# Optimization experiments

Measured on AMD Instinct MI355X. Metric: run time of the kernel, lower is better.

Reference implementation:

```python
import jax, jax.numpy as jnp
import numpy as np

B, NC, PY, PX = 1, 2, 32, 32
DIM, HEADS = 1024, 16
IMAGE_H = IMAGE_W = 448
FREQ_BASE = 100.0


def _so3_exp(w):
    # w: (..., 3) axis-angle -> (..., 3, 3) rotation (Rodrigues)
    theta = jnp.maximum(jnp.linalg.norm(w, axis=-1, keepdims=True)[..., None], 1e-8)
    wx, wy, wz = w[..., 0], w[..., 1], w[..., 2]
    z = jnp.zeros_like(wx)
    K = jnp.stack([jnp.stack([z, -wz, wy], -1),
                   jnp.stack([wz, z, -wx], -1),
                   jnp.stack([-wy, wx, z], -1)], -2)
    A = jnp.sin(theta) / theta
    Bc = (1.0 - jnp.cos(theta)) / (theta * theta)
    return jnp.eye(3) + A * K + Bc * (K @ K)


def setup_inputs() -> dict:
    key = jax.random.key(0)
    ks = jax.random.split(key, 6)
    N = NC * PY * PX
    x = jax.random.normal(ks[0], (B, N, DIM), jnp.float32)
    # SE(3) camera extrinsics (world-to-camera)
    R = _so3_exp(0.2 * jax.random.normal(ks[1], (B, NC, 3), jnp.float32))
    t = 0.5 * jax.random.normal(ks[2], (B, NC, 3), jnp.float32)
    ext = jnp.zeros((B, NC, 4, 4), jnp.float32)
    ext = ext.at[..., :3, :3].set(R).at[..., :3, 3].set(t).at[..., 3, 3].set(1.0)
    f = 500.0
    Ks = jnp.zeros((B, NC, 3, 3), jnp.float32)
    Ks = (Ks.at[..., 0, 0].set(f).at[..., 1, 1].set(f)
            .at[..., 0, 2].set(IMAGE_W / 2.0).at[..., 1, 2].set(IMAGE_H / 2.0)
            .at[..., 2, 2].set(1.0))
    s = 1.0 / np.sqrt(DIM)
    qkv_w = s * jax.random.normal(ks[3], (3 * DIM, DIM), jnp.float32)
    proj_w = s * jax.random.normal(ks[4], (DIM, DIM), jnp.float32)
    proj_b = jnp.zeros((DIM,), jnp.float32)
    return dict(x=x, extrinsics=ext, Ks=Ks, qkv_w=qkv_w, proj_w=proj_w, proj_b=proj_b,
                image_h=IMAGE_H, image_w=IMAGE_W, patch_h=PY, patch_w=PX)


def _prope_attention(x, extrinsics, Ks, qkv_w, proj_w, proj_b,
                     image_h, image_w, patch_h, patch_w):
    Bb, N, C = x.shape
    H = HEADS
    D = C // H
    nc = extrinsics.shape[1]
    n_per = patch_h * patch_w  # tokens per camera

    # ---- QKV projection ----
    qkv = (x @ qkv_w.T).reshape(Bb, N, 3, H, D).transpose(0, 3, 2, 1, 4)  # B,H,3,N,D
    q, k, v = qkv[:, :, 0], qkv[:, :, 1], qkv[:, :, 2]

    # ---- per-camera normalized projection matrices P = K_norm(4x4) @ viewmat ----
    sx, sy = 2.0 / image_w, 2.0 / image_h  # pixel -> NDC-ish normalization
    Kn = jnp.zeros(Ks.shape[:-2] + (4, 4), x.dtype)
    Kn = (Kn.at[..., 0, 0].set(Ks[..., 0, 0] * sx)
            .at[..., 1, 1].set(Ks[..., 1, 1] * sy)
            .at[..., 0, 2].set(Ks[..., 0, 2] * sx - 1.0)
            .at[..., 1, 2].set(Ks[..., 1, 2] * sy - 1.0)
            .at[..., 2, 2].set(1.0).at[..., 3, 3].set(1.0))
    P = Kn @ extrinsics                      # (B, nc, 4, 4)
    P_inv = jnp.linalg.inv(P)

    def per_token(M):  # (B,nc,4,4) -> (B,N,4,4), broadcast camera over its tokens
        return jnp.repeat(M, n_per, axis=1)

    Mq = per_token(jnp.swapaxes(P_inv, -1, -2))  # P_i^{-T}
    Mk = per_token(P)                            # P_j
    Mo = per_token(P_inv)                        # P_i^{-1}

    # ---- channel split: half projective (blocks of 4), half 2D RoPE ----
    d_proj = D // 2
    d_rope = D - d_proj
    nf = d_rope // 4  # frequencies per axis (pairs of channels)
    freqs = FREQ_BASE ** (-jnp.arange(nf, dtype=x.dtype) / nf)
    ysg, xsg = jnp.meshgrid(jnp.arange(patch_h), jnp.arange(patch_w), indexing='ij')
    pos_x = jnp.tile(xsg.reshape(-1), nc).astype(x.dtype)  # (N,)
    pos_y = jnp.tile(ysg.reshape(-1), nc).astype(x.dtype)
    ang = jnp.concatenate([pos_x[:, None] * freqs, pos_y[:, None] * freqs], -1)  # (N, 2nf)
    cos, sin = jnp.cos(ang), jnp.sin(ang)

    def apply(t, M, sign):
        lead = t.shape[:-1]  # (B,H,N)
        tp = t[..., :d_proj].reshape(lead + (d_proj // 4, 4))
        tp = jnp.einsum('bnij,bhnkj->bhnki', M, tp).reshape(lead + (d_proj,))
        tr = t[..., d_proj:].reshape(lead + (2 * nf, 2))
        a, b = tr[..., 0], tr[..., 1]
        s = sign * sin
        tr = jnp.stack([a * cos - b * s, a * s + b * cos], -1).reshape(lead + (d_rope,))
        return jnp.concatenate([tp, tr], -1)

    q = apply(q, Mq, 1.0)
    k = apply(k, Mk, 1.0)
    v = apply(v, Mk, 1.0)

    # ---- SDPA ----
    scale = 1.0 / np.sqrt(D)
    attn = jax.nn.softmax(jnp.einsum('bhqd,bhkd->bhqk', q, k) * scale, axis=-1)
    out = jnp.einsum('bhqk,bhkd->bhqd', attn, v)

    # ---- inverse output transform ----
    out = apply(out, Mo, -1.0)
    out = out.transpose(0, 2, 1, 3).reshape(Bb, N, C)
    return out @ proj_w.T + proj_b


def reference(x, extrinsics, Ks, qkv_w, proj_w, proj_b, image_h, image_w, patch_h, patch_w):
    return _prope_attention(x, extrinsics, Ks, qkv_w, proj_w, proj_b,
                            image_h, image_w, patch_h, patch_w)
```

## Files before the change

kernel.cpp:

```cpp
#include <hip/hip_runtime.h>
#include <math.h>

#define N_TOK   2048
#define DIM     1024
#define HEADS   16
#define HD      64
#define NCAMS   2
#define NPER    1024
#define DPROJ   32
#define NF      8
#define KSPLIT  4

#define LOG2E   1.44269504088896340736f

typedef _Float16 half8  __attribute__((ext_vector_type(8)));
typedef _Float16 half4h __attribute__((ext_vector_type(4)));
typedef _Float16 half2h __attribute__((ext_vector_type(2)));
typedef __fp16   fp16x2 __attribute__((ext_vector_type(2)));
typedef float    floatx4 __attribute__((ext_vector_type(4)));

#define MATS_OFF  0
#define WPROJ_OFF 256
#define SCR_OFF   (WPROJ_OFF + 524288)
#define XF_OFF    (SCR_OFF)
#define WQKV_OFF  (SCR_OFF + 1048576)
#define QKV16_OFF (SCR_OFF + 2621440)
#define OP_OFF    (SCR_OFF)
#define ML_OFF    (SCR_OFF + 4194304)
#define Q_OFF     (SCR_OFF + 5767168)
#define K_OFF     (Q_OFF + 1048576)
#define V_OFF     (K_OFF + 1048576)
#define OT_OFF    (V_OFF + 1048576)

__device__ __forceinline__ void gl_lds16(const void* g, void* s) {
    __builtin_amdgcn_global_load_lds((const __attribute__((address_space(1))) void*)g,
                                     (__attribute__((address_space(3))) void*)s, 16, 0, 0);
}

__global__ __launch_bounds__(256) void cast_and_mats(const float* __restrict__ x,
                                                     const float* __restrict__ wqkv,
                                                     const float* __restrict__ wproj,
                                                     const float* __restrict__ ext,
                                                     const float* __restrict__ Ksm,
                                                     _Float16* __restrict__ xf,
                                                     _Float16* __restrict__ wqkvf,
                                                     _Float16* __restrict__ wprojf,
                                                     float* __restrict__ mats) {
    size_t i = ((size_t)blockIdx.x * 256 + threadIdx.x) * 8;
    const float* src; _Float16* dst; size_t off;
    if (i < (size_t)2*1024*1024)       { src = x;     dst = xf;     off = i; }
    else if (i < (size_t)5*1024*1024)  { src = wqkv;  dst = wqkvf;  off = i - (size_t)2*1024*1024; }
    else                               { src = wproj; dst = wprojf; off = i - (size_t)5*1024*1024; }
    float4 a = *(const float4*)(src + off);
    float4 b = *(const float4*)(src + off + 4);
    half8 h;
    h[0] = (_Float16)a.x; h[1] = (_Float16)a.y; h[2] = (_Float16)a.z; h[3] = (_Float16)a.w;
    h[4] = (_Float16)b.x; h[5] = (_Float16)b.y; h[6] = (_Float16)b.z; h[7] = (_Float16)b.w;
    *(half8*)(dst + off) = h;

    if (blockIdx.x == 0 && threadIdx.x < NCAMS) {
        const int c = threadIdx.x;
        const float sx = 2.0f / 448.0f, sy = 2.0f / 448.0f;
        const float* Kc = Ksm + c * 9;
        const float* E  = ext + c * 16;
        float Kn[16];
#pragma unroll
        for (int t = 0; t < 16; t++) Kn[t] = 0.0f;
        Kn[0]  = Kc[0] * sx;
        Kn[2]  = Kc[2] * sx - 1.0f;
        Kn[5]  = Kc[4] * sy;
        Kn[6]  = Kc[5] * sy - 1.0f;
        Kn[10] = 1.0f; Kn[15] = 1.0f;
        float P[16];
#pragma unroll
        for (int r = 0; r < 4; r++)
#pragma unroll
            for (int cc = 0; cc < 4; cc++) {
                float s = 0.0f;
#pragma unroll
                for (int k = 0; k < 4; k++) s += Kn[r*4+k] * E[k*4+cc];
                P[r*4+cc] = s;
            }
        float M[4][8];
        for (int r = 0; r < 4; r++)
            for (int cc = 0; cc < 4; cc++) { M[r][cc] = P[r*4+cc]; M[r][4+cc] = (r==cc) ? 1.0f : 0.0f; }
        for (int col = 0; col < 4; col++) {
            int piv = col;
            for (int r = col+1; r < 4; r++)
                if (fabsf(M[r][col]) > fabsf(M[piv][col])) piv = r;
            if (piv != col)
                for (int j = 0; j < 8; j++) { float tmp = M[col][j]; M[col][j] = M[piv][j]; M[piv][j] = tmp; }
            float d = 1.0f / M[col][col];
            for (int j = 0; j < 8; j++) M[col][j] *= d;
            for (int r = 0; r < 4; r++) {
                if (r == col) continue;
                float f = M[r][col];
                for (int j = 0; j < 8; j++) M[r][j] -= f * M[col][j];
            }
        }
        float Pi[16];
        for (int r = 0; r < 4; r++)
            for (int cc = 0; cc < 4; cc++) Pi[r*4+cc] = M[r][4+cc];
        float* o = mats + c * 48;
        for (int r = 0; r < 4; r++)
            for (int cc = 0; cc < 4; cc++) o[r*4+cc] = Pi[cc*4+r];
        for (int t = 0; t < 16; t++) o[16+t] = P[t];
        for (int t = 0; t < 16; t++) o[32+t] = Pi[t];
    }
}

template <bool F16OUT>
__global__ __launch_bounds__(256) void gemm_mfma(const _Float16* __restrict__ A,
                                                 const _Float16* __restrict__ Bw,
                                                 const float* __restrict__ bias,
                                                 void* __restrict__ C,
                                                 int Nn, int Kd) {
    __shared__ _Float16 As[2][64 * 32];
    __shared__ _Float16 Bs[2][128 * 32];
    const int tid  = threadIdx.x;
    const int w    = tid >> 6, lane = tid & 63;
    const int ql   = lane & 15, quad = lane >> 4;
    const int lr   = lane >> 2, lc = lane & 3;
    const int row0 = blockIdx.y * 64, col0 = blockIdx.x * 128;

    floatx4 acc[4][2];
#pragma unroll
    for (int mt = 0; mt < 4; mt++)
#pragma unroll
        for (int nt = 0; nt < 2; nt++) acc[mt][nt] = (floatx4){0.f, 0.f, 0.f, 0.f};

    const _Float16* Ab  = A  + (size_t)(row0 + w * 16 + lr) * Kd + lc * 8;
    const _Float16* Bb0 = Bw + (size_t)(col0 + w * 32 + lr) * Kd + lc * 8;
    const _Float16* Bb1 = Bw + (size_t)(col0 + w * 32 + 16 + lr) * Kd + lc * 8;

    gl_lds16(Ab,  &As[0][(w * 16) * 32]);
    gl_lds16(Bb0, &Bs[0][(w * 32) * 32]);
    gl_lds16(Bb1, &Bs[0][(w * 32 + 16) * 32]);

    const int nIter = Kd >> 5;
    for (int i = 0; i < nIter; i++) {
        __syncthreads();
        if (i + 1 < nIter) {
            const int k0 = (i + 1) << 5;
            const int nb = (i + 1) & 1;
            gl_lds16(Ab + k0,  &As[nb][(w * 16) * 32]);
            gl_lds16(Bb0 + k0, &Bs[nb][(w * 32) * 32]);
            gl_lds16(Bb1 + k0, &Bs[nb][(w * 32 + 16) * 32]);
        }
        const int cur = i & 1;
        half8 af[4], bf[2];
#pragma unroll
        for (int mt = 0; mt < 4; mt++)
            af[mt] = *(const half8*)&As[cur][(mt * 16 + ql) * 32 + quad * 8];
#pragma unroll
        for (int nt = 0; nt < 2; nt++)
            bf[nt] = *(const half8*)&Bs[cur][(w * 32 + nt * 16 + ql) * 32 + quad * 8];
#pragma unroll
        for (int mt = 0; mt < 4; mt++)
#pragma unroll
            for (int nt = 0; nt < 2; nt++)
                acc[mt][nt] = __builtin_amdgcn_mfma_f32_16x16x32_f16(af[mt], bf[nt], acc[mt][nt], 0, 0, 0);
    }

#pragma unroll
    for (int nt = 0; nt < 2; nt++) {
        const int col = col0 + w * 32 + nt * 16 + ql;
        float bb = F16OUT ? 0.0f : bias[col];
#pragma unroll
        for (int mt = 0; mt < 4; mt++) {
            const int row = row0 + mt * 16 + quad * 4;
            if (F16OUT) {
                _Float16* Cp = (_Float16*)C;
#pragma unroll
                for (int r = 0; r < 4; r++)
                    Cp[(size_t)(row + r) * Nn + col] = (_Float16)acc[mt][nt][r];
            } else {
                float* Cp = (float*)C;
#pragma unroll
                for (int r = 0; r < 4; r++)
                    Cp[(size_t)(row + r) * Nn + col] = acc[mt][nt][r] + bb;
            }
        }
    }
}

__global__ __launch_bounds__(256) void transform_qkv(const _Float16* __restrict__ qkv,
                                                     const float* __restrict__ mats,
                                                     _Float16* __restrict__ Qf,
                                                     _Float16* __restrict__ Kf,
                                                     _Float16* __restrict__ Vtf) {
    const bool isV = blockIdx.x >= 2048;
    int n, h, sub, s;
    if (!isV) {
        const int T = blockIdx.x * 256 + threadIdx.x;
        sub = T & 7; h = (T >> 3) & 15; s = (T >> 7) & 1; n = T >> 8;
    } else {
        const int u = (blockIdx.x - 2048) * 256 + threadIdx.x;
        const int nl = u & 63;
        sub = (u >> 6) & 7; h = (u >> 9) & 15; n = (u >> 13) * 64 + nl; s = 2;
    }

    half8 v = *(const half8*)&qkv[(size_t)n * (3*DIM) + s * DIM + h * HD + sub * 8];
    float t[8];
#pragma unroll
    for (int i = 0; i < 8; i++) t[i] = (float)v[i];

    const int cam = n >> 10;
    const float* A = mats + cam * 48 + (s == 0 ? 0 : 16);
    float r[8];
    if (sub < 4) {
#pragma unroll
        for (int g = 0; g < 2; g++)
#pragma unroll
            for (int i = 0; i < 4; i++)
                r[g*4+i] = A[i*4+0]*t[g*4+0] + A[i*4+1]*t[g*4+1]
                         + A[i*4+2]*t[g*4+2] + A[i*4+3]*t[g*4+3];
    } else {
        const int p = n & (NPER - 1);
        const float px = (float)(p & 31), py = (float)(p >> 5);
        const int pt0 = (sub - 4) * 4;
#pragma unroll
        for (int pp = 0; pp < 4; pp++) {
            const int pt = pt0 + pp;
            const float fr = __expf(-0.5756462732485114f * (float)(pt & 7));
            const float ang = (pt < NF ? px : py) * fr;
            float sn, cs; __sincosf(ang, &sn, &cs);
            const float a = t[pp*2], b = t[pp*2+1];
            r[pp*2]   = a * cs - b * sn;
            r[pp*2+1] = a * sn + b * cs;
        }
    }

    if (s == 0) {
        half8 o;
#pragma unroll
        for (int i = 0; i < 8; i++) o[i] = (_Float16)(r[i] * (0.125f * LOG2E));
        *(half8*)&Qf[((size_t)h * N_TOK + n) * HD + sub * 8] = o;
    } else if (s == 1) {
        half8 o;
#pragma unroll
        for (int i = 0; i < 8; i++) o[i] = (_Float16)r[i];
        *(half8*)&Kf[((size_t)h * N_TOK + n) * HD + sub * 8] = o;
    } else {
#pragma unroll
        for (int i = 0; i < 8; i++)
            Vtf[(size_t)(h * HD + sub * 8 + i) * N_TOK + n] = (_Float16)r[i];
    }
}

#define PLD 68
__global__ __launch_bounds__(256) void attn_mfma(const _Float16* __restrict__ Qh,
                                                 const _Float16* __restrict__ Kh,
                                                 const _Float16* __restrict__ Vt,
                                                 _Float16* __restrict__ OP,
                                                 float* __restrict__ ML) {
    __shared__ _Float16 sK[64 * 64];
    __shared__ _Float16 sV[64 * 64];
    __shared__ _Float16 P_lds[4][16][PLD];
    const int w    = threadIdx.x >> 6;
    const int lane = threadIdx.x & 63;
    const int b  = blockIdx.x;
    const int ks = b >> 9;
    const int hh = (b >> 5) & 15;
    const int qb = b & 31;
    const int ql = lane & 15, quad = lane >> 4;
    const int q0 = qb * 64 + w * 16;

    const int srow = lane >> 3;
    const int schk = (lane & 7) ^ srow;
    const int c0 = ((quad ^ (ql & 7)) << 3);
    const int c1 = c0 ^ 32;

    const _Float16* Qp = Qh + ((size_t)hh * N_TOK + q0 + ql) * HD;
    const half8 qf0 = *(const half8*)(Qp + quad * 8);
    const half8 qf1 = *(const half8*)(Qp + 32 + quad * 8);

    const _Float16* Kb = Kh + (size_t)hh * N_TOK * HD;
    const _Float16* Vb = Vt + (size_t)hh * HD * N_TOK;

    floatx4 O[4];
#pragma unroll
    for (int mt = 0; mt < 4; mt++) O[mt] = (floatx4){0.f, 0.f, 0.f, 0.f};
    float m = -1e30f, l = 0.0f;

    const int kstart = ks * (N_TOK / KSPLIT);
    const int nIter  = (N_TOK / KSPLIT) / 64;

    for (int i = 0; i < nIter; i++) {
        const int kb = kstart + i * 64;
#pragma unroll
        for (int j = 0; j < 2; j++) {
            const int r0 = w * 16 + j * 8;
            gl_lds16(Kb + (size_t)(kb + r0 + srow) * HD + schk * 8, &sK[r0 * 64]);
            gl_lds16(Vb + (size_t)(r0 + srow) * N_TOK + kb + schk * 8, &sV[r0 * 64]);
        }
        __syncthreads();
        floatx4 s[4];
#pragma unroll
        for (int kt = 0; kt < 4; kt++) {
            const int rb = (kt * 16 + ql) * 64;
            half8 ka0 = *(const half8*)&sK[rb + c0];
            half8 ka1 = *(const half8*)&sK[rb + c1];
            floatx4 acc = (floatx4){0.f, 0.f, 0.f, 0.f};
            acc = __builtin_amdgcn_mfma_f32_16x16x32_f16(ka0, qf0, acc, 0, 0, 0);
            acc = __builtin_amdgcn_mfma_f32_16x16x32_f16(ka1, qf1, acc, 0, 0, 0);
            s[kt] = acc;
        }
        float bm = -1e30f;
#pragma unroll
        for (int kt = 0; kt < 4; kt++)
#pragma unroll
            for (int r = 0; r < 4; r++) bm = fmaxf(bm, s[kt][r]);
        bm = fmaxf(bm, __shfl_xor(bm, 16, 64));
        bm = fmaxf(bm, __shfl_xor(bm, 32, 64));
        const float mnew = fmaxf(m, bm);
        if (__ballot(bm > m)) {
            const float alpha = exp2f(m - mnew);
            l *= alpha;
#pragma unroll
            for (int mt = 0; mt < 4; mt++)
#pragma unroll
                for (int r = 0; r < 4; r++) O[mt][r] *= alpha;
        }
        m = mnew;
        float p[4][4];
        float ps = 0.0f;
#pragma unroll
        for (int kt = 0; kt < 4; kt++)
#pragma unroll
            for (int r = 0; r < 4; r++) { p[kt][r] = exp2f(s[kt][r] - mnew); ps += p[kt][r]; }
        l += ps;
#pragma unroll
        for (int kt = 0; kt < 4; kt++) {
            union { fp16x2 h; half2h v; } u01, u23;
            u01.h = __builtin_amdgcn_cvt_pkrtz(p[kt][0], p[kt][1]);
            u23.h = __builtin_amdgcn_cvt_pkrtz(p[kt][2], p[kt][3]);
            *(half2h*)&P_lds[w][ql][kt * 16 + quad * 4]     = u01.v;
            *(half2h*)&P_lds[w][ql][kt * 16 + quad * 4 + 2] = u23.v;
        }
        union { half8 v8; half4h v4[2]; } pu0, pu1;
        pu0.v4[0] = *(const half4h*)&P_lds[w][ql][quad * 8];
        pu0.v4[1] = *(const half4h*)&P_lds[w][ql][quad * 8 + 4];
        pu1.v4[0] = *(const half4h*)&P_lds[w][ql][32 + quad * 8];
        pu1.v4[1] = *(const half4h*)&P_lds[w][ql][32 + quad * 8 + 4];
#pragma unroll
        for (int mt = 0; mt < 4; mt++) {
            const int rb = (mt * 16 + ql) * 64;
            half8 va0 = *(const half8*)&sV[rb + c0];
            half8 va1 = *(const half8*)&sV[rb + c1];
            O[mt] = __builtin_amdgcn_mfma_f32_16x16x32_f16(va0, pu0.v8, O[mt], 0, 0, 0);
            O[mt] = __builtin_amdgcn_mfma_f32_16x16x32_f16(va1, pu1.v8, O[mt], 0, 0, 0);
        }
        __syncthreads();
    }
    l += __shfl_xor(l, 16, 64);
    l += __shfl_xor(l, 32, 64);
    const float rl = 1.0f / l;
    _Float16* Op = OP + (((size_t)(ks * HEADS + hh)) * N_TOK + q0 + ql) * HD;
#pragma unroll
    for (int mt = 0; mt < 4; mt++) {
        half4h o4;
#pragma unroll
        for (int r = 0; r < 4; r++) o4[r] = (_Float16)(O[mt][r] * rl);
        *(half4h*)&Op[mt * 16 + quad * 4] = o4;
    }
    if (quad == 0) {
        float2 mlv = {m, l};
        *(float2*)&ML[(((size_t)(ks * HEADS + hh)) * N_TOK + q0 + ql) * 2] = mlv;
    }
}

__global__ __launch_bounds__(256) void transform_out(const _Float16* __restrict__ OP,
                                                     const float* __restrict__ ML,
                                                     const float* __restrict__ mats,
                                                     _Float16* __restrict__ Ot) {
    const int T = blockIdx.x * 256 + threadIdx.x;
    const int sub = T & 7;
    const int h   = (T >> 3) & 15;
    const int n   = T >> 7;

    half8 op[KSPLIT];
    float2 ml[KSPLIT];
#pragma unroll
    for (int i = 0; i < KSPLIT; i++) {
        op[i] = *(const half8*)&OP[(((size_t)(i * HEADS + h)) * N_TOK + n) * HD + sub * 8];
        ml[i] = *(const float2*)&ML[(((size_t)(i * HEADS + h)) * N_TOK + n) * 2];
    }
    float mstar = ml[0].x;
#pragma unroll
    for (int i = 1; i < KSPLIT; i++) mstar = fmaxf(mstar, ml[i].x);
    float W = 0.0f;
    float t[8] = {0.f, 0.f, 0.f, 0.f, 0.f, 0.f, 0.f, 0.f};
#pragma unroll
    for (int i = 0; i < KSPLIT; i++) {
        const float wgt = exp2f(ml[i].x - mstar) * ml[i].y;
        W += wgt;
#pragma unroll
        for (int d = 0; d < 8; d++) t[d] += wgt * (float)op[i][d];
    }
    const float rW = 1.0f / W;
#pragma unroll
    for (int d = 0; d < 8; d++) t[d] *= rW;

    const int cam = n >> 10;
    const float* A = mats + cam * 48 + 32;
    float r[8];
    if (sub < 4) {
#pragma unroll
        for (int g = 0; g < 2; g++)
#pragma unroll
            for (int i = 0; i < 4; i++)
                r[g*4+i] = A[i*4+0]*t[g*4+0] + A[i*4+1]*t[g*4+1]
                         + A[i*4+2]*t[g*4+2] + A[i*4+3]*t[g*4+3];
    } else {
        const int p = n & (NPER - 1);
        const float px = (float)(p & 31), py = (float)(p >> 5);
        const int pt0 = (sub - 4) * 4;
#pragma unroll
        for (int pp = 0; pp < 4; pp++) {
            const int pt = pt0 + pp;
            const float fr = __expf(-0.5756462732485114f * (float)(pt & 7));
            const float ang = (pt < NF ? px : py) * fr;
            float sn, cs; __sincosf(ang, &sn, &cs);
            const float a = t[pp*2], b = t[pp*2+1];
            r[pp*2]   = a * cs + b * sn;
            r[pp*2+1] = -a * sn + b * cs;
        }
    }
    half8 o;
#pragma unroll
    for (int i = 0; i < 8; i++) o[i] = (_Float16)r[i];
    *(half8*)&Ot[(size_t)n * DIM + h * HD + sub * 8] = o;
}

extern "C" void kernel_launch(void* const* d_in, const int* in_sizes, int n_in,
                              void* d_out, int out_size, void* d_ws, size_t ws_size,
                              hipStream_t stream) {
    const float* x      = (const float*)d_in[0];
    const float* ext    = (const float*)d_in[1];
    const float* Ks     = (const float*)d_in[2];
    const float* qkv_w  = (const float*)d_in[3];
    const float* proj_w = (const float*)d_in[4];
    const float* proj_b = (const float*)d_in[5];
    float* out = (float*)d_out;

    float* ws   = (float*)d_ws;
    float* mats = ws + MATS_OFF;
    _Float16* Wprojf = (_Float16*)(ws + WPROJ_OFF);
    _Float16* Xf     = (_Float16*)(ws + XF_OFF);
    _Float16* Wqkvf  = (_Float16*)(ws + WQKV_OFF);
    _Float16* qkv16  = (_Float16*)(ws + QKV16_OFF);
    _Float16* OP     = (_Float16*)(ws + OP_OFF);
    float*    ML     = ws + ML_OFF;
    _Float16* Qf  = (_Float16*)(ws + Q_OFF);
    _Float16* Kf  = (_Float16*)(ws + K_OFF);
    _Float16* Vtf = (_Float16*)(ws + V_OFF);
    _Float16* Ot16 = (_Float16*)(ws + OT_OFF);

    cast_and_mats<<<3072, 256, 0, stream>>>(x, qkv_w, proj_w, ext, Ks,
                                            Xf, Wqkvf, Wprojf, mats);

    gemm_mfma<true><<<dim3(3*DIM/128, N_TOK/64), 256, 0, stream>>>(
        Xf, Wqkvf, nullptr, (void*)qkv16, 3*DIM, DIM);

    transform_qkv<<<3072, 256, 0, stream>>>(qkv16, mats, Qf, Kf, Vtf);

    attn_mfma<<<KSPLIT * HEADS * (N_TOK / 64), 256, 0, stream>>>(Qf, Kf, Vtf, OP, ML);

    transform_out<<<N_TOK * HEADS * 8 / 256, 256, 0, stream>>>(OP, ML, mats, Ot16);

    gemm_mfma<false><<<dim3(DIM/128, N_TOK/64), 256, 0, stream>>>(
        Ot16, Wprojf, proj_b, (void*)out, DIM, DIM);
}
```

Baseline: 185.3 us.

## Fuse PRoPE q/k/v transform into QKV GEMM epilogue and halve attention k-split

Result: no change. 183.5 us (-1.0%).

```diff
diff --git a/kernel.cpp b/kernel.cpp
--- a/kernel.cpp
+++ b/kernel.cpp
@@ -9,7 +9,7 @@
 #define NPER    1024
 #define DPROJ   32
 #define NF      8
-#define KSPLIT  4
+#define KSPLIT  2
 
 #define LOG2E   1.44269504088896340736f
 
@@ -24,9 +24,8 @@
 #define SCR_OFF   (WPROJ_OFF + 524288)
 #define XF_OFF    (SCR_OFF)
 #define WQKV_OFF  (SCR_OFF + 1048576)
-#define QKV16_OFF (SCR_OFF + 2621440)
-#define OP_OFF    (SCR_OFF)
-#define ML_OFF    (SCR_OFF + 4194304)
+#define OP_OFF    (SCR_OFF + 2621440)
+#define ML_OFF    (SCR_OFF + 4718592)
 #define Q_OFF     (SCR_OFF + 5767168)
 #define K_OFF     (Q_OFF + 1048576)
 #define V_OFF     (K_OFF + 1048576)
@@ -109,12 +108,13 @@
     }
 }
 
-template <bool F16OUT>
-__global__ __launch_bounds__(256) void gemm_mfma(const _Float16* __restrict__ A,
-                                                 const _Float16* __restrict__ Bw,
-                                                 const float* __restrict__ bias,
-                                                 void* __restrict__ C,
-                                                 int Nn, int Kd) {
+__global__ __launch_bounds__(256) void gemm_qkv_fused(const _Float16* __restrict__ A,
+                                                      const _Float16* __restrict__ Bw,
+                                                      const float* __restrict__ mats,
+                                                      _Float16* __restrict__ Qf,
+                                                      _Float16* __restrict__ Kf,
+                                                      _Float16* __restrict__ Vtf) {
+    const int Kd = DIM, Nn = 3*DIM;
     __shared__ _Float16 As[2][64 * 32];
     __shared__ _Float16 Bs[2][128 * 32];
     const int tid  = threadIdx.x;
@@ -162,89 +162,136 @@
                 acc[mt][nt] = __builtin_amdgcn_mfma_f32_16x16x32_f16(af[mt], bf[nt], acc[mt][nt], 0, 0, 0);
     }
 
+    const int s   = col0 >> 10;
+    const int cam = row0 >> 10;
+    const float* Amat = mats + cam * 48 + (s == 0 ? 0 : 16);
+    const int i4 = (ql & 3) * 4;
+    const float A0 = Amat[i4+0], A1 = Amat[i4+1], A2 = Amat[i4+2], A3 = Amat[i4+3];
+    const int g = lane & ~3;
+    const float sc = (s == 0) ? 0.125f * LOG2E : 1.0f;
+
+#pragma unroll
+    for (int nt = 0; nt < 2; nt++) {
+        const int cb = col0 + w * 32 + nt * 16;
+        const int dbase = cb & 63;
+        const int d = dbase + ql;
+        const int h = (cb >> 6) & 15;
+        float out[4][4];
+        if (dbase < 32) {
+#pragma unroll
+            for (int mt = 0; mt < 4; mt++)
+#pragma unroll
+                for (int r = 0; r < 4; r++) {
+                    const float v  = acc[mt][nt][r];
+                    const float t0 = __shfl(v, g + 0, 64);
+                    const float t1 = __shfl(v, g + 1, 64);
+                    const float t2 = __shfl(v, g + 2, 64);
+                    const float t3 = __shfl(v, g + 3, 64);
+                    out[mt][r] = A0*t0 + A1*t1 + A2*t2 + A3*t3;
+                }
+        } else {
+            const int pt = (d - 32) >> 1;
+            const float fr = __expf(-0.5756462732485114f * (float)(pt & 7));
+            const bool usex = (pt < NF);
+#pragma unroll
+            for (int mt = 0; mt < 4; mt++)
+#pragma unroll
+                for (int r = 0; r < 4; r++) {
+                    const float v = acc[mt][nt][r];
+                    const float other = __shfl_xor(v, 1, 64);
+                    const int n = row0 + mt * 16 + quad * 4 + r;
+                    const int p = n & (NPER - 1);
+                    const float pos = (float)(usex ? (p & 31) : (p >> 5));
+                    float sn, cs; __sincosf(pos * fr, &sn, &cs);
+                    const float sgn = (d & 1) ? sn : -sn;
+                    out[mt][r] = v * cs + other * sgn;
+                }
+        }
+        if (s < 2) {
+            _Float16* dst = (s == 0) ? Qf : Kf;
+#pragma unroll
+            for (int mt = 0; mt < 4; mt++)
+#pragma unroll
+                for (int r = 0; r < 4; r++) {
+                    const int n = row0 + mt * 16 + quad * 4 + r;
+                    dst[((size_t)h * N_TOK + n) * HD + d] = (_Float16)(out[mt][r] * sc);
+                }
+        } else {
+#pragma unroll
+            for (int mt = 0; mt < 4; mt++) {
+                half4h o4;
+#pragma unroll
+                for (int r = 0; r < 4; r++) o4[r] = (_Float16)out[mt][r];
+                const int n0 = row0 + mt * 16 + quad * 4;
+                *(half4h*)&Vtf[((size_t)h * HD + d) * N_TOK + n0] = o4;
+            }
+        }
+    }
+}
+
+__global__ __launch_bounds__(256) void gemm_proj(const _Float16* __restrict__ A,
+                                                 const _Float16* __restrict__ Bw,
+                                                 const float* __restrict__ bias,
+                                                 float* __restrict__ C,
+                                                 int Nn, int Kd) {
+    __shared__ _Float16 As[2][64 * 32];
+    __shared__ _Float16 Bs[2][128 * 32];
+    const int tid  = threadIdx.x;
+    const int w    = tid >> 6, lane = tid & 63;
+    const int ql   = lane & 15, quad = lane >> 4;
+    const int lr   = lane >> 2, lc = lane & 3;
+    const int row0 = blockIdx.y * 64, col0 = blockIdx.x * 128;
+
+    floatx4 acc[4][2];
+#pragma unroll
+    for (int mt = 0; mt < 4; mt++)
+#pragma unroll
+        for (int nt = 0; nt < 2; nt++) acc[mt][nt] = (floatx4){0.f, 0.f, 0.f, 0.f};
+
+    const _Float16* Ab  = A  + (size_t)(row0 + w * 16 + lr) * Kd + lc * 8;
+    const _Float16* Bb0 = Bw + (size_t)(col0 + w * 32 + lr) * Kd + lc * 8;
+    const _Float16* Bb1 = Bw + (size_t)(col0 + w * 32 + 16 + lr) * Kd + lc * 8;
+
+    gl_lds16(Ab,  &As[0][(w * 16) * 32]);
+    gl_lds16(Bb0, &Bs[0][(w * 32) * 32]);
+    gl_lds16(Bb1, &Bs[0][(w * 32 + 16) * 32]);
+
+    const int nIter = Kd >> 5;
+    for (int i = 0; i < nIter; i++) {
+        __syncthreads();
+        if (i + 1 < nIter) {
+            const int k0 = (i + 1) << 5;
+            const int nb = (i + 1) & 1;
+            gl_lds16(Ab + k0,  &As[nb][(w * 16) * 32]);
+            gl_lds16(Bb0 + k0, &Bs[nb][(w * 32) * 32]);
+            gl_lds16(Bb1 + k0, &Bs[nb][(w * 32 + 16) * 32]);
+        }
+        const int cur = i & 1;
+        half8 af[4], bf[2];
+#pragma unroll
+        for (int mt = 0; mt < 4; mt++)
+            af[mt] = *(const half8*)&As[cur][(mt * 16 + ql) * 32 + quad * 8];
+#pragma unroll
+        for (int nt = 0; nt < 2; nt++)
+            bf[nt] = *(const half8*)&Bs[cur][(w * 32 + nt * 16 + ql) * 32 + quad * 8];
+#pragma unroll
+        for (int mt = 0; mt < 4; mt++)
+#pragma unroll
+            for (int nt = 0; nt < 2; nt++)
+                acc[mt][nt] = __builtin_amdgcn_mfma_f32_16x16x32_f16(af[mt], bf[nt], acc[mt][nt], 0, 0, 0);
+    }
+
 #pragma unroll
     for (int nt = 0; nt < 2; nt++) {
         const int col = col0 + w * 32 + nt * 16 + ql;
-        float bb = F16OUT ? 0.0f : bias[col];
+        const float bb = bias[col];
 #pragma unroll
         for (int mt = 0; mt < 4; mt++) {
             const int row = row0 + mt * 16 + quad * 4;
-            if (F16OUT) {
-                _Float16* Cp = (_Float16*)C;
-#pragma unroll
-                for (int r = 0; r < 4; r++)
-                    Cp[(size_t)(row + r) * Nn + col] = (_Float16)acc[mt][nt][r];
-            } else {
-                float* Cp = (float*)C;
-#pragma unroll
-                for (int r = 0; r < 4; r++)
-                    Cp[(size_t)(row + r) * Nn + col] = acc[mt][nt][r] + bb;
-            }
-        }
-    }
-}
-
-__global__ __launch_bounds__(256) void transform_qkv(const _Float16* __restrict__ qkv,
-                                                     const float* __restrict__ mats,
-                                                     _Float16* __restrict__ Qf,
-                                                     _Float16* __restrict__ Kf,
-                                                     _Float16* __restrict__ Vtf) {
-    const bool isV = blockIdx.x >= 2048;
-    int n, h, sub, s;
-    if (!isV) {
-        const int T = blockIdx.x * 256 + threadIdx.x;
-        sub = T & 7; h = (T >> 3) & 15; s = (T >> 7) & 1; n = T >> 8;
-    } else {
-        const int u = (blockIdx.x - 2048) * 256 + threadIdx.x;
-        const int nl = u & 63;
-        sub = (u >> 6) & 7; h = (u >> 9) & 15; n = (u >> 13) * 64 + nl; s = 2;
-    }
-
-    half8 v = *(const half8*)&qkv[(size_t)n * (3*DIM) + s * DIM + h * HD + sub * 8];
-    float t[8];
-#pragma unroll
-    for (int i = 0; i < 8; i++) t[i] = (float)v[i];
-
-    const int cam = n >> 10;
-    const float* A = mats + cam * 48 + (s == 0 ? 0 : 16);
-    float r[8];
-    if (sub < 4) {
-#pragma unroll
-        for (int g = 0; g < 2; g++)
-#pragma unroll
-            for (int i = 0; i < 4; i++)
-                r[g*4+i] = A[i*4+0]*t[g*4+0] + A[i*4+1]*t[g*4+1]
-                         + A[i*4+2]*t[g*4+2] + A[i*4+3]*t[g*4+3];
-    } else {
-        const int p = n & (NPER - 1);
-        const float px = (float)(p & 31), py = (float)(p >> 5);
-        const int pt0 = (sub - 4) * 4;
-#pragma unroll
-        for (int pp = 0; pp < 4; pp++) {
-            const int pt = pt0 + pp;
-            const float fr = __expf(-0.5756462732485114f * (float)(pt & 7));
-            const float ang = (pt < NF ? px : py) * fr;
-            float sn, cs; __sincosf(ang, &sn, &cs);
-            const float a = t[pp*2], b = t[pp*2+1];
-            r[pp*2]   = a * cs - b * sn;
-            r[pp*2+1] = a * sn + b * cs;
-        }
-    }
-
-    if (s == 0) {
-        half8 o;
-#pragma unroll
-        for (int i = 0; i < 8; i++) o[i] = (_Float16)(r[i] * (0.125f * LOG2E));
-        *(half8*)&Qf[((size_t)h * N_TOK + n) * HD + sub * 8] = o;
-    } else if (s == 1) {
-        half8 o;
-#pragma unroll
-        for (int i = 0; i < 8; i++) o[i] = (_Float16)r[i];
-        *(half8*)&Kf[((size_t)h * N_TOK + n) * HD + sub * 8] = o;
-    } else {
-#pragma unroll
-        for (int i = 0; i < 8; i++)
-            Vtf[(size_t)(h * HD + sub * 8 + i) * N_TOK + n] = (_Float16)r[i];
+#pragma unroll
+            for (int r = 0; r < 4; r++)
+                C[(size_t)(row + r) * Nn + col] = acc[mt][nt][r] + bb;
+        }
     }
 }
 
@@ -449,7 +496,6 @@
     _Float16* Wprojf = (_Float16*)(ws + WPROJ_OFF);
     _Float16* Xf     = (_Float16*)(ws + XF_OFF);
     _Float16* Wqkvf  = (_Float16*)(ws + WQKV_OFF);
-    _Float16* qkv16  = (_Float16*)(ws + QKV16_OFF);
     _Float16* OP     = (_Float16*)(ws + OP_OFF);
     float*    ML     = ws + ML_OFF;
     _Float16* Qf  = (_Float16*)(ws + Q_OFF);
@@ -460,15 +506,13 @@
     cast_and_mats<<<3072, 256, 0, stream>>>(x, qkv_w, proj_w, ext, Ks,
                                             Xf, Wqkvf, Wprojf, mats);
 
-    gemm_mfma<true><<<dim3(3*DIM/128, N_TOK/64), 256, 0, stream>>>(
-        Xf, Wqkvf, nullptr, (void*)qkv16, 3*DIM, DIM);
-
-    transform_qkv<<<3072, 256, 0, stream>>>(qkv16, mats, Qf, Kf, Vtf);
+    gemm_qkv_fused<<<dim3(3*DIM/128, N_TOK/64), 256, 0, stream>>>(
+        Xf, Wqkvf, mats, Qf, Kf, Vtf);
 
     attn_mfma<<<KSPLIT * HEADS * (N_TOK / 64), 256, 0, stream>>>(Qf, Kf, Vtf, OP, ML);
 
     transform_out<<<N_TOK * HEADS * 8 / 256, 256, 0, stream>>>(OP, ML, mats, Ot16);
 
-    gemm_mfma<false><<<dim3(DIM/128, N_TOK/64), 256, 0, stream>>>(
-        Ot16, Wprojf, proj_b, (void*)out, DIM, DIM);
-}
+    gemm_proj<<<dim3(DIM/128, N_TOK/64), 256, 0, stream>>>(
+        Ot16, Wprojf, proj_b, out, DIM, DIM);
+}
```
